# Kernel tuning notes

Hardware: AMD Instinct MI355X
Metric: run time of the kernel (lower is better)

Reference implementation:

```python
import jax, jax.numpy as jnp
import numpy as np

DIM = 512
HEADS = 8
DK = DIM // HEADS
MAX_LEN = 22118
EPS = 1e-5


def _layernorm(h, g, b):
    m = jnp.mean(h, axis=-1, keepdims=True)
    v = jnp.mean((h - m) ** 2, axis=-1, keepdims=True)
    return (h - m) / jnp.sqrt(v + EPS) * g + b


def setup_inputs() -> dict:
    key = jax.random.key(0)
    ks = jax.random.split(key, 16)
    B, S = 4, 2048
    xavier = lambda k, shp: jax.random.normal(k, shp, jnp.float32) * np.sqrt(2.0 / (shp[0] + shp[1]))
    return {
        "x": jax.random.normal(ks[0], (B, S, DIM), jnp.float32),
        "vis_data": jax.random.normal(ks[1], (B, S, DIM), jnp.float32),
        "coord1": jax.random.randint(ks[2], (B, S), 0, MAX_LEN, jnp.int32),
        "coord2": jax.random.randint(ks[3], (B, S), 0, MAX_LEN, jnp.int32),
        "emb1": jax.random.normal(ks[4], (MAX_LEN, DIM // 2), jnp.float32) * 0.02,
        "emb2": jax.random.normal(ks[5], (MAX_LEN, DIM // 2), jnp.float32) * 0.02,
        "wq": xavier(ks[6], (DIM, DIM)), "bq": jnp.zeros((DIM,), jnp.float32),
        "wk": xavier(ks[7], (DIM, DIM)), "bk": jnp.zeros((DIM,), jnp.float32),
        "wv": xavier(ks[8], (DIM, DIM)), "bv": jnp.zeros((DIM,), jnp.float32),
        "w1": xavier(ks[9], (DIM, DIM)), "b1": jnp.zeros((DIM,), jnp.float32),
        "g1": jnp.ones((DIM,), jnp.float32), "beta1": jnp.zeros((DIM,), jnp.float32),
        "w2": xavier(ks[10], (DIM, DIM)), "b2": jnp.zeros((DIM,), jnp.float32),
        "g2": jnp.ones((DIM,), jnp.float32), "beta2": jnp.zeros((DIM,), jnp.float32),
    }


def reference(x, vis_data, coord1, coord2, emb1, emb2, wq, bq, wk, bk, wv, bv,
              w1, b1, g1, beta1, w2, b2, g2, beta2):
    B, S, _ = x.shape
    # learned positional encoding: concat of two coordinate embeddings
    pos = jnp.concatenate([emb1[coord1], emb2[coord2]], axis=-1)  # [B,S,DIM]
    xp = x + pos
    # Q/K from vis_data, V from position-encoded x
    q = (vis_data @ wq + bq).reshape(B, S, HEADS, DK)
    k = (vis_data @ wk + bk).reshape(B, S, HEADS, DK)
    v = (xp @ wv + bv).reshape(B, S, HEADS, DK)
    scores = jnp.einsum("bqhd,bkhd->bhqk", q, k) / np.sqrt(DK).astype(np.float32)
    attn = jax.nn.softmax(scores, axis=-1)  # dropout is identity in eval
    out = jnp.einsum("bhqk,bkhd->bqhd", attn, v).reshape(B, S, DIM)
    # post-attention MLP stack (self.layer)
    h = jax.nn.leaky_relu(out @ w1 + b1, negative_slope=0.2)
    h = _layernorm(h, g1, beta1)
    h = jax.nn.leaky_relu(h @ w2 + b2, negative_slope=0.2)
    h = _layernorm(h, g2, beta2)
    return h
```

## Files before the change

kernel.cpp:

```cpp
#include <hip/hip_runtime.h>

#define DIM 512
#define SEQ 2048
#define MROWS 8192

typedef short short8 __attribute__((ext_vector_type(8)));
typedef float floatx4 __attribute__((ext_vector_type(4)));

__device__ __forceinline__ ushort f2bf(float f) {
  union { float f; unsigned u; } v; v.f = f;
  unsigned r = v.u + 0x7fff + ((v.u >> 16) & 1);
  return (ushort)(r >> 16);
}
__device__ __forceinline__ float bf2f(ushort u) {
  union { unsigned u; float f; } v; v.u = ((unsigned)u) << 16;
  return v.f;
}
__device__ __forceinline__ float fast_exp2(float x) {
  float r;
  asm("v_exp_f32 %0, %1" : "=v"(r) : "v"(x));
  return r;
}

__global__ __launch_bounds__(256) void prep_wtrans_kernel(
    const float* __restrict__ x, const float* __restrict__ vis,
    const int* __restrict__ c1, const int* __restrict__ c2,
    const float* __restrict__ e1, const float* __restrict__ e2,
    const float* __restrict__ wq, const float* __restrict__ wk,
    const float* __restrict__ wv, const float* __restrict__ w1,
    const float* __restrict__ w2,
    ushort* __restrict__ xp_bf, ushort* __restrict__ vis_bf,
    ushort* __restrict__ wt_qkv, ushort* __restrict__ wt1,
    ushort* __restrict__ wt2) {
  __shared__ float Ls[64 * 65];
  if (blockIdx.x < 4096) {
    int gid = blockIdx.x * 256 + threadIdx.x;
    int row = gid >> 7;
    int col = (gid & 127) * 4;
    float4 vv = *(const float4*)(vis + (size_t)row * 512 + col);
    ushort4 vb; vb.x = f2bf(vv.x); vb.y = f2bf(vv.y); vb.z = f2bf(vv.z); vb.w = f2bf(vv.w);
    *(ushort4*)(vis_bf + (size_t)row * 512 + col) = vb;
    float4 p;
    if (col < 256) p = *(const float4*)(e1 + (size_t)c1[row] * 256 + col);
    else           p = *(const float4*)(e2 + (size_t)c2[row] * 256 + col - 256);
    float4 xv = *(const float4*)(x + (size_t)row * 512 + col);
    ushort4 xb; xb.x = f2bf(xv.x + p.x); xb.y = f2bf(xv.y + p.y);
    xb.z = f2bf(xv.z + p.z); xb.w = f2bf(xv.w + p.w);
    *(ushort4*)(xp_bf + (size_t)row * 512 + col) = xb;
  } else {
    int bid = blockIdx.x - 4096;
    int mid = bid >> 6;
    int tile = bid & 63;
    int k0 = (tile >> 3) * 64, n0 = (tile & 7) * 64;
    const float* W = mid == 0 ? wq : mid == 1 ? wk : mid == 2 ? wv : mid == 3 ? w1 : w2;
    ushort* outp = mid < 3 ? (wt_qkv + (size_t)mid * 512 * 512) : (mid == 3 ? wt1 : wt2);
    float scale = (mid == 0) ? 0.125f * 1.44269504f : 1.0f;
    int r = threadIdx.x >> 4, c4 = (threadIdx.x & 15) * 4;
#pragma unroll
    for (int i = 0; i < 4; i++) {
      int row = i * 16 + r;
      float4 wv4 = *(const float4*)(W + (size_t)(k0 + row) * 512 + n0 + c4);
      Ls[row * 65 + c4 + 0] = wv4.x * scale;
      Ls[row * 65 + c4 + 1] = wv4.y * scale;
      Ls[row * 65 + c4 + 2] = wv4.z * scale;
      Ls[row * 65 + c4 + 3] = wv4.w * scale;
    }
    __syncthreads();
    int n = threadIdx.x >> 2, kc = (threadIdx.x & 3) * 16;
    ushort pk[16];
#pragma unroll
    for (int i = 0; i < 16; i++) pk[i] = f2bf(Ls[(kc + i) * 65 + n]);
    ushort* op = outp + (size_t)(n0 + n) * 512 + k0 + kc;
    *(uint4*)op = *(uint4*)pk;
    *(uint4*)(op + 8) = *(uint4*)(pk + 8);
  }
}

template <bool LEAKY>
__global__ __launch_bounds__(256, 4) void gemm_mfma(
    const ushort* __restrict__ A01, const ushort* __restrict__ A2,
    const ushort* __restrict__ Wt,
    const float* __restrict__ bias0, const float* __restrict__ bias1,
    const float* __restrict__ bias2,
    ushort* __restrict__ out0, ushort* __restrict__ out1,
    ushort* __restrict__ out2, float s0scale) {
  __shared__ __align__(16) ushort Sm[24576];
  int t = threadIdx.x;
  int seg = blockIdx.x >> 2;
  int nloc0 = (blockIdx.x & 3) * 128;
  int n0w = blockIdx.x * 128;
  int m0 = blockIdx.y * 64;
  const ushort* A = (seg < 2) ? A01 : A2;
  const float* bias = seg == 0 ? bias0 : seg == 1 ? bias1 : bias2;
  ushort* out = seg == 0 ? out0 : seg == 1 ? out1 : out2;
  float bscale = seg == 0 ? s0scale : 1.0f;

  int w = t >> 6, lane = t & 63;
  int wm = (w & 1) * 32, wn = (w >> 1) * 64;
  int quad = lane >> 4, lcol = lane & 15;
  int l8g = lane >> 3, l7g = lane & 7;
  int gchs = (l7g ^ l8g) * 8;

  floatx4 acc[2][4] = {};

#define GEMM_STAGE(K0, BUF)                                                   \
  {                                                                           \
    ushort* As_ = Sm + (BUF) * 12288;                                         \
    ushort* Bs_ = As_ + 4096;                                                 \
    _Pragma("unroll") for (int i = 0; i < 2; i++) {                           \
      int r0 = w * 16 + i * 8;                                                \
      __builtin_amdgcn_global_load_lds(                                       \
          (const __attribute__((address_space(1))) unsigned*)(                \
              A + (size_t)(m0 + r0 + l8g) * 512 + (K0) + gchs),               \
          (__attribute__((address_space(3))) unsigned*)(&As_[r0 * 64]),       \
          16, 0, 0);                                                          \
    }                                                                         \
    _Pragma("unroll") for (int i = 0; i < 4; i++) {                           \
      int r0 = w * 32 + i * 8;                                                \
      __builtin_amdgcn_global_load_lds(                                       \
          (const __attribute__((address_space(1))) unsigned*)(                \
              Wt + (size_t)(n0w + r0 + l8g) * 512 + (K0) + gchs),             \
          (__attribute__((address_space(3))) unsigned*)(&Bs_[r0 * 64]),       \
          16, 0, 0);                                                          \
    }                                                                         \
  }

  GEMM_STAGE(0, 0);
  asm volatile("s_waitcnt vmcnt(0)" ::: "memory");
  __syncthreads();

  for (int ks = 0; ks < 8; ks++) {
    int cur = ks & 1;
    if (ks < 7) GEMM_STAGE((ks + 1) * 64, cur ^ 1);
    const ushort* As = Sm + cur * 12288;
    const ushort* Bs = As + 4096;
#pragma unroll
    for (int kc = 0; kc < 2; kc++) {
      int pch = ((kc * 4 + quad) ^ (lcol & 7)) * 8;
      short8 af[2], bfr[4];
#pragma unroll
      for (int i = 0; i < 2; i++)
        af[i] = *(const short8*)(&As[(wm + i * 16 + lcol) * 64 + pch]);
#pragma unroll
      for (int i = 0; i < 4; i++)
        bfr[i] = *(const short8*)(&Bs[(wn + i * 16 + lcol) * 64 + pch]);
#pragma unroll
      for (int mt = 0; mt < 2; mt++)
#pragma unroll
        for (int nt = 0; nt < 4; nt++)
          acc[mt][nt] = __builtin_amdgcn_mfma_f32_16x16x32_bf16(
              af[mt], bfr[nt], acc[mt][nt], 0, 0, 0);
    }
    asm volatile("s_waitcnt vmcnt(0)" ::: "memory");
    __syncthreads();
  }
#undef GEMM_STAGE

  float* Ls = (float*)Sm + w * 1088;
  int rr = lane >> 2, cc = (lane & 3) * 16;
#pragma unroll
  for (int mt = 0; mt < 2; mt++) {
#pragma unroll
    for (int nt = 0; nt < 4; nt++) {
      float bv = bias[nloc0 + wn + nt * 16 + lcol] * bscale;
#pragma unroll
      for (int r = 0; r < 4; r++) {
        float vv = acc[mt][nt][r] + bv;
        if (LEAKY) vv = vv >= 0.f ? vv : 0.2f * vv;
        Ls[(quad * 4 + r) * 68 + nt * 16 + lcol] = vv;
      }
    }
    asm volatile("s_waitcnt lgkmcnt(0)" ::: "memory");
    ushort pk[16];
#pragma unroll
    for (int i = 0; i < 16; i += 4) {
      float4 fv = *(const float4*)(&Ls[rr * 68 + cc + i]);
      pk[i] = f2bf(fv.x); pk[i + 1] = f2bf(fv.y);
      pk[i + 2] = f2bf(fv.z); pk[i + 3] = f2bf(fv.w);
    }
    ushort* op = out + (size_t)(m0 + wm + mt * 16 + rr) * 512 + nloc0 + wn + cc;
    *(uint4*)op = *(uint4*)pk;
    *(uint4*)(op + 8) = *(uint4*)(pk + 8);
    asm volatile("s_waitcnt lgkmcnt(0)" ::: "memory");
  }
}

__global__ __launch_bounds__(256, 4) void attn_mfma_kernel(
    const ushort* __restrict__ q, const ushort* __restrict__ k,
    const ushort* __restrict__ v, ushort* __restrict__ out) {
  __shared__ __align__(16) ushort Ks[2][64 * 64];
  __shared__ __align__(16) ushort Vt[2][64 * 64];
  __shared__ __align__(16) unsigned Pp[2048];
  int t = threadIdx.x;
  int blk = blockIdx.x;
  blk = ((blk & 7) << 7) | (blk >> 3);
  int qt = blk & 31, h = (blk >> 5) & 7, b = blk >> 8;
  int wave = t >> 6, lane = t & 63, quad = lane >> 4, lcol = lane & 15;
  int q0 = qt * 64 + wave * 16;
  const size_t base = (size_t)b * SEQ * 512 + h * 64;

  short8 qf[2];
#pragma unroll
  for (int kc = 0; kc < 2; kc++)
    qf[kc] = *(const short8*)(
        q + base + (size_t)(q0 + lcol) * 512 + kc * 32 + quad * 8);

  floatx4 O[4] = {};
  float lsum = 0.f;

  unsigned* Ppw = Pp + wave * 512;
  int l8 = lane >> 3, l7 = lane & 7;
  int kchs = (l7 ^ l8) * 8;
  int krow = wave * 8 + l8;
  int vp = t & 31, vdg = t >> 5;
  const ushort* vbase = v + base + (size_t)(2 * vp) * 512 + vdg * 8;

  uint4 ka0, ka1, va, vb;

  ka0 = *(const uint4*)(k + base + (size_t)krow * 512 + kchs);
  ka1 = *(const uint4*)(k + base + (size_t)(krow + 32) * 512 + kchs);
  va = *(const uint4*)vbase;
  vb = *(const uint4*)(vbase + 512);
  *(uint4*)(&Ks[0][krow * 64 + l7 * 8]) = ka0;
  *(uint4*)(&Ks[0][(krow + 32) * 64 + l7 * 8]) = ka1;
  {
    const ushort* a0 = (const ushort*)&va;
    const ushort* a1 = (const ushort*)&vb;
#pragma unroll
    for (int i = 0; i < 8; i++) {
      int dim = vdg * 8 + i;
      unsigned pack = (unsigned)a0[i] | ((unsigned)a1[i] << 16);
      *(unsigned*)(&Vt[0][dim * 64 + ((vp >> 2) ^ (dim & 7)) * 8 +
                          (vp & 3) * 2]) = pack;
    }
  }
  __syncthreads();

  int cb = 0;
  for (int it = 0; it < 32; it++) {
    if (it < 31) {
      int ktn = (it + 1) * 64;
      ka0 = *(const uint4*)(k + base + (size_t)(ktn + krow) * 512 + kchs);
      ka1 = *(const uint4*)(k + base + (size_t)(ktn + krow + 32) * 512 + kchs);
      const ushort* vr = vbase + (size_t)ktn * 512;
      va = *(const uint4*)vr;
      vb = *(const uint4*)(vr + 512);
    }

    const ushort* Ksb = Ks[cb];
    const ushort* Vtb = Vt[cb];

    short8 kf[2][4];
#pragma unroll
    for (int kc = 0; kc < 2; kc++) {
      int pch = ((kc * 4 + quad) ^ l7) * 8;
#pragma unroll
      for (int jt = 0; jt < 4; jt++)
        kf[kc][jt] = *(const short8*)(&Ksb[(jt * 16 + lcol) * 64 + pch]);
    }
    floatx4 S[4] = {};
    __builtin_amdgcn_s_setprio(1);
#pragma unroll
    for (int kc = 0; kc < 2; kc++)
#pragma unroll
      for (int jt = 0; jt < 4; jt++)
        S[jt] = __builtin_amdgcn_mfma_f32_16x16x32_bf16(
            kf[kc][jt], qf[kc], S[jt], 0, 0, 0);
    __builtin_amdgcn_s_setprio(0);

#pragma unroll
    for (int jt = 0; jt < 4; jt++) {
      float e0 = fast_exp2(S[jt][0]);
      float e1 = fast_exp2(S[jt][1]);
      float e2 = fast_exp2(S[jt][2]);
      float e3 = fast_exp2(S[jt][3]);
      lsum += (e0 + e1) + (e2 + e3);
      unsigned p0, p1;
      asm("v_cvt_pk_bf16_f32 %0, %1, %2" : "=v"(p0) : "v"(e0), "v"(e1));
      asm("v_cvt_pk_bf16_f32 %0, %1, %2" : "=v"(p1) : "v"(e2), "v"(e3));
      int c0 = 2 * jt + (quad >> 1);
      uint2 pk2; pk2.x = p0; pk2.y = p1;
      *(uint2*)(Ppw + lcol * 32 + ((c0 ^ l7) << 2) + (quad & 1) * 2) = pk2;
    }
    asm volatile("s_waitcnt lgkmcnt(0)" ::: "memory");

#pragma unroll
    for (int kc = 0; kc < 2; kc++) {
      short8 vf[4];
      int ch = ((kc * 4 + quad) ^ l7) * 8;
#pragma unroll
      for (int nt = 0; nt < 4; nt++)
        vf[nt] = *(const short8*)(&Vtb[(nt * 16 + lcol) * 64 + ch]);
      short8 pf = *(const short8*)(Ppw + lcol * 32 +
                                   (((kc * 4 + quad) ^ l7) << 2));
      __builtin_amdgcn_s_setprio(1);
#pragma unroll
      for (int nt = 0; nt < 4; nt++)
        O[nt] = __builtin_amdgcn_mfma_f32_16x16x32_bf16(
            vf[nt], pf, O[nt], 0, 0, 0);
      __builtin_amdgcn_s_setprio(0);
    }

    if (it < 31) {
      ushort* Ksn = Ks[cb ^ 1];
      *(uint4*)(&Ksn[krow * 64 + l7 * 8]) = ka0;
      *(uint4*)(&Ksn[(krow + 32) * 64 + l7 * 8]) = ka1;
      const ushort* a0 = (const ushort*)&va;
      const ushort* a1 = (const ushort*)&vb;
      ushort* Vtn = Vt[cb ^ 1];
#pragma unroll
      for (int i = 0; i < 8; i++) {
        int dim = vdg * 8 + i;
        unsigned pack = (unsigned)a0[i] | ((unsigned)a1[i] << 16);
        *(unsigned*)(&Vtn[dim * 64 + ((vp >> 2) ^ (dim & 7)) * 8 +
                          (vp & 3) * 2]) = pack;
      }
    }
    __syncthreads();
    cb ^= 1;
  }

  lsum += __shfl_xor(lsum, 16, 64);
  lsum += __shfl_xor(lsum, 32, 64);
  float rl = 1.f / lsum;
#pragma unroll
  for (int nt = 0; nt < 4; nt++) {
    ushort4 o;
    o.x = f2bf(O[nt][0] * rl);
    o.y = f2bf(O[nt][1] * rl);
    o.z = f2bf(O[nt][2] * rl);
    o.w = f2bf(O[nt][3] * rl);
    *(ushort4*)(out + base + (size_t)(q0 + lcol) * 512 + nt * 16 + quad * 4) = o;
  }
}

template <bool OUTF32>
__global__ __launch_bounds__(256) void ln_kernel(
    const ushort* __restrict__ h, const float* __restrict__ g,
    const float* __restrict__ beta, void* __restrict__ outv) {
  int wave = threadIdx.x >> 6, lane = threadIdx.x & 63;
  int row = blockIdx.x * 4 + wave;
  uint4 raw = *(const uint4*)(h + (size_t)row * 512 + lane * 8);
  const ushort* hu = (const ushort*)&raw;
  float vals[8];
#pragma unroll
  for (int i = 0; i < 8; i++) vals[i] = bf2f(hu[i]);
  float sum = 0.f;
#pragma unroll
  for (int i = 0; i < 8; i++) sum += vals[i];
#pragma unroll
  for (int off = 32; off >= 1; off >>= 1) sum += __shfl_xor(sum, off, 64);
  float mean = sum * (1.f / 512.f);
  float vs = 0.f;
#pragma unroll
  for (int i = 0; i < 8; i++) { float d = vals[i] - mean; vs += d * d; }
#pragma unroll
  for (int off = 32; off >= 1; off >>= 1) vs += __shfl_xor(vs, off, 64);
  float rstd = rsqrtf(vs * (1.f / 512.f) + 1e-5f);
  float4 gv0 = *(const float4*)(g + lane * 8);
  float4 gv1 = *(const float4*)(g + lane * 8 + 4);
  float4 bv0 = *(const float4*)(beta + lane * 8);
  float4 bv1 = *(const float4*)(beta + lane * 8 + 4);
  float gr[8] = {gv0.x, gv0.y, gv0.z, gv0.w, gv1.x, gv1.y, gv1.z, gv1.w};
  float br[8] = {bv0.x, bv0.y, bv0.z, bv0.w, bv1.x, bv1.y, bv1.z, bv1.w};
  float res[8];
#pragma unroll
  for (int i = 0; i < 8; i++) res[i] = (vals[i] - mean) * rstd * gr[i] + br[i];
  if (OUTF32) {
    float* op = (float*)outv + (size_t)row * 512 + lane * 8;
    float4 o0, o1;
    o0.x = res[0]; o0.y = res[1]; o0.z = res[2]; o0.w = res[3];
    o1.x = res[4]; o1.y = res[5]; o1.z = res[6]; o1.w = res[7];
    *(float4*)op = o0; *(float4*)(op + 4) = o1;
  } else {
    ushort* op = (ushort*)outv + (size_t)row * 512 + lane * 8;
    ushort4 o0, o1;
    o0.x = f2bf(res[0]); o0.y = f2bf(res[1]); o0.z = f2bf(res[2]); o0.w = f2bf(res[3]);
    o1.x = f2bf(res[4]); o1.y = f2bf(res[5]); o1.z = f2bf(res[6]); o1.w = f2bf(res[7]);
    *(ushort4*)op = o0; *(ushort4*)(op + 4) = o1;
  }
}

extern "C" void kernel_launch(void* const* d_in, const int* in_sizes, int n_in,
                              void* d_out, int out_size, void* d_ws,
                              size_t ws_size, hipStream_t stream) {
  (void)in_sizes; (void)n_in; (void)out_size; (void)ws_size;
  const float* x     = (const float*)d_in[0];
  const float* vis   = (const float*)d_in[1];
  const int*   c1    = (const int*)d_in[2];
  const int*   c2    = (const int*)d_in[3];
  const float* e1    = (const float*)d_in[4];
  const float* e2    = (const float*)d_in[5];
  const float* wq    = (const float*)d_in[6];
  const float* bq    = (const float*)d_in[7];
  const float* wk    = (const float*)d_in[8];
  const float* bk    = (const float*)d_in[9];
  const float* wv    = (const float*)d_in[10];
  const float* bv    = (const float*)d_in[11];
  const float* w1    = (const float*)d_in[12];
  const float* b1    = (const float*)d_in[13];
  const float* g1    = (const float*)d_in[14];
  const float* beta1 = (const float*)d_in[15];
  const float* w2    = (const float*)d_in[16];
  const float* b2    = (const float*)d_in[17];
  const float* g2    = (const float*)d_in[18];
  const float* beta2 = (const float*)d_in[19];
  float* out = (float*)d_out;
  ushort* ws = (ushort*)d_ws;

  const size_t BUF = (size_t)MROWS * 512;
  ushort* xp_bf  = ws;
  ushort* vis_bf = ws + BUF;
  ushort* q_bf   = ws + 2 * BUF;
  ushort* k_bf   = ws + 3 * BUF;
  ushort* v_bf   = ws + 4 * BUF;
  ushort* wt_qkv = ws + 5 * BUF;
  ushort* wt1    = wt_qkv + 1536 * 512;
  ushort* wt2    = wt1 + 512 * 512;
  ushort* attn_bf = vis_bf;
  ushort* h1_bf   = xp_bf;
  ushort* ln1_bf  = q_bf;
  ushort* h2_bf   = k_bf;

  prep_wtrans_kernel<<<4416, 256, 0, stream>>>(
      x, vis, c1, c2, e1, e2, wq, wk, wv, w1, w2, xp_bf, vis_bf, wt_qkv, wt1, wt2);
  gemm_mfma<false><<<dim3(12, 128), 256, 0, stream>>>(
      vis_bf, xp_bf, wt_qkv, bq, bk, bv, q_bf, k_bf, v_bf, 0.125f * 1.44269504f);
  attn_mfma_kernel<<<1024, 256, 0, stream>>>(q_bf, k_bf, v_bf, attn_bf);
  gemm_mfma<true><<<dim3(4, 128), 256, 0, stream>>>(
      attn_bf, attn_bf, wt1, b1, b1, b1, h1_bf, h1_bf, h1_bf, 1.0f);
  ln_kernel<false><<<2048, 256, 0, stream>>>(h1_bf, g1, beta1, ln1_bf);
  gemm_mfma<true><<<dim3(4, 128), 256, 0, stream>>>(
      ln1_bf, ln1_bf, wt2, b2, b2, b2, h2_bf, h2_bf, h2_bf, 1.0f);
  ln_kernel<true><<<2048, 256, 0, stream>>>(h2_bf, g2, beta2, out);
}
```

Before: 248.2 us.

## Enlarge GEMM tile to 128x128 and drop double buffering

The GEMM kernel's M tile grows from 64 to 128 rows, so each wave now computes a 64x64 output block with 4x4 accumulators and the grid halves along M. The LDS double buffer is replaced by a single buffer, with a wait and barrier before each k-step's compute. The aim is more operand reuse per loaded tile and fewer blocks. In exchange, global loads no longer overlap with MFMA work, register pressure rises (launch bounds go from 4 to 3), and the three GEMMs launch fewer blocks (768 and 256).

After: 260.7 us. +5.0%, slower.

```diff
diff --git a/kernel.cpp b/kernel.cpp
--- a/kernel.cpp
+++ b/kernel.cpp
@@ -77,89 +77,80 @@
 }
 
 template <bool LEAKY>
-__global__ __launch_bounds__(256, 4) void gemm_mfma(
+__global__ __launch_bounds__(256, 3) void gemm_mfma(
     const ushort* __restrict__ A01, const ushort* __restrict__ A2,
     const ushort* __restrict__ Wt,
     const float* __restrict__ bias0, const float* __restrict__ bias1,
     const float* __restrict__ bias2,
     ushort* __restrict__ out0, ushort* __restrict__ out1,
     ushort* __restrict__ out2, float s0scale) {
-  __shared__ __align__(16) ushort Sm[24576];
+  __shared__ __align__(16) ushort Sm[16384];
+  ushort* As = Sm;
+  ushort* Bs = Sm + 8192;
   int t = threadIdx.x;
   int seg = blockIdx.x >> 2;
   int nloc0 = (blockIdx.x & 3) * 128;
   int n0w = blockIdx.x * 128;
-  int m0 = blockIdx.y * 64;
+  int m0 = blockIdx.y * 128;
   const ushort* A = (seg < 2) ? A01 : A2;
   const float* bias = seg == 0 ? bias0 : seg == 1 ? bias1 : bias2;
   ushort* out = seg == 0 ? out0 : seg == 1 ? out1 : out2;
   float bscale = seg == 0 ? s0scale : 1.0f;
 
   int w = t >> 6, lane = t & 63;
-  int wm = (w & 1) * 32, wn = (w >> 1) * 64;
+  int wm = (w & 1) * 64, wn = (w >> 1) * 64;
   int quad = lane >> 4, lcol = lane & 15;
   int l8g = lane >> 3, l7g = lane & 7;
   int gchs = (l7g ^ l8g) * 8;
 
-  floatx4 acc[2][4] = {};
-
-#define GEMM_STAGE(K0, BUF)                                                   \
-  {                                                                           \
-    ushort* As_ = Sm + (BUF) * 12288;                                         \
-    ushort* Bs_ = As_ + 4096;                                                 \
-    _Pragma("unroll") for (int i = 0; i < 2; i++) {                           \
-      int r0 = w * 16 + i * 8;                                                \
-      __builtin_amdgcn_global_load_lds(                                       \
-          (const __attribute__((address_space(1))) unsigned*)(                \
-              A + (size_t)(m0 + r0 + l8g) * 512 + (K0) + gchs),               \
-          (__attribute__((address_space(3))) unsigned*)(&As_[r0 * 64]),       \
-          16, 0, 0);                                                          \
-    }                                                                         \
-    _Pragma("unroll") for (int i = 0; i < 4; i++) {                           \
-      int r0 = w * 32 + i * 8;                                                \
-      __builtin_amdgcn_global_load_lds(                                       \
-          (const __attribute__((address_space(1))) unsigned*)(                \
-              Wt + (size_t)(n0w + r0 + l8g) * 512 + (K0) + gchs),             \
-          (__attribute__((address_space(3))) unsigned*)(&Bs_[r0 * 64]),       \
-          16, 0, 0);                                                          \
-    }                                                                         \
-  }
-
-  GEMM_STAGE(0, 0);
-  asm volatile("s_waitcnt vmcnt(0)" ::: "memory");
-  __syncthreads();
+  floatx4 acc[4][4] = {};
 
   for (int ks = 0; ks < 8; ks++) {
-    int cur = ks & 1;
-    if (ks < 7) GEMM_STAGE((ks + 1) * 64, cur ^ 1);
-    const ushort* As = Sm + cur * 12288;
-    const ushort* Bs = As + 4096;
+    int k0 = ks * 64;
+#pragma unroll
+    for (int i = 0; i < 4; i++) {
+      int r0 = w * 32 + i * 8;
+      __builtin_amdgcn_global_load_lds(
+          (const __attribute__((address_space(1))) unsigned*)(
+              A + (size_t)(m0 + r0 + l8g) * 512 + k0 + gchs),
+          (__attribute__((address_space(3))) unsigned*)(&As[r0 * 64]),
+          16, 0, 0);
+    }
+#pragma unroll
+    for (int i = 0; i < 4; i++) {
+      int r0 = w * 32 + i * 8;
+      __builtin_amdgcn_global_load_lds(
+          (const __attribute__((address_space(1))) unsigned*)(
+              Wt + (size_t)(n0w + r0 + l8g) * 512 + k0 + gchs),
+          (__attribute__((address_space(3))) unsigned*)(&Bs[r0 * 64]),
+          16, 0, 0);
+    }
+    asm volatile("s_waitcnt vmcnt(0)" ::: "memory");
+    __syncthreads();
 #pragma unroll
     for (int kc = 0; kc < 2; kc++) {
       int pch = ((kc * 4 + quad) ^ (lcol & 7)) * 8;
-      short8 af[2], bfr[4];
-#pragma unroll
-      for (int i = 0; i < 2; i++)
+      short8 af[4], bfr[4];
+#pragma unroll
+      for (int i = 0; i < 4; i++)
         af[i] = *(const short8*)(&As[(wm + i * 16 + lcol) * 64 + pch]);
 #pragma unroll
       for (int i = 0; i < 4; i++)
         bfr[i] = *(const short8*)(&Bs[(wn + i * 16 + lcol) * 64 + pch]);
 #pragma unroll
-      for (int mt = 0; mt < 2; mt++)
+      for (int mt = 0; mt < 4; mt++)
 #pragma unroll
         for (int nt = 0; nt < 4; nt++)
           acc[mt][nt] = __builtin_amdgcn_mfma_f32_16x16x32_bf16(
               af[mt], bfr[nt], acc[mt][nt], 0, 0, 0);
     }
-    asm volatile("s_waitcnt vmcnt(0)" ::: "memory");
     __syncthreads();
   }
-#undef GEMM_STAGE
 
   float* Ls = (float*)Sm + w * 1088;
   int rr = lane >> 2, cc = (lane & 3) * 16;
 #pragma unroll
-  for (int mt = 0; mt < 2; mt++) {
+  for (int mt = 0; mt < 4; mt++) {
 #pragma unroll
     for (int nt = 0; nt < 4; nt++) {
       float bv = bias[nloc0 + wn + nt * 16 + lcol] * bscale;
@@ -424,13 +415,13 @@
 
   prep_wtrans_kernel<<<4416, 256, 0, stream>>>(
       x, vis, c1, c2, e1, e2, wq, wk, wv, w1, w2, xp_bf, vis_bf, wt_qkv, wt1, wt2);
-  gemm_mfma<false><<<dim3(12, 128), 256, 0, stream>>>(
+  gemm_mfma<false><<<dim3(12, 64), 256, 0, stream>>>(
       vis_bf, xp_bf, wt_qkv, bq, bk, bv, q_bf, k_bf, v_bf, 0.125f * 1.44269504f);
   attn_mfma_kernel<<<1024, 256, 0, stream>>>(q_bf, k_bf, v_bf, attn_bf);
-  gemm_mfma<true><<<dim3(4, 128), 256, 0, stream>>>(
+  gemm_mfma<true><<<dim3(4, 64), 256, 0, stream>>>(
       attn_bf, attn_bf, wt1, b1, b1, b1, h1_bf, h1_bf, h1_bf, 1.0f);
   ln_kernel<false><<<2048, 256, 0, stream>>>(h1_bf, g1, beta1, ln1_bf);
-  gemm_mfma<true><<<dim3(4, 128), 256, 0, stream>>>(
+  gemm_mfma<true><<<dim3(4, 64), 256, 0, stream>>>(
       ln1_bf, ln1_bf, wt2, b2, b2, b2, h2_bf, h2_bf, h2_bf, 1.0f);
   ln_kernel<true><<<2048, 256, 0, stream>>>(h2_bf, g2, beta2, out);
 }
```

## Fuse first layernorm into GEMM epilogue stats and next GEMM A-load

Applied to the files above, without the earlier changes.

Removes the standalone first layernorm kernel. The first MLP GEMM epilogue now accumulates per-row sum and sum-of-squares via shuffles and atomics into a stats buffer, which the prep kernel zeroes. The second GEMM normalizes its A tile on the fly from those stats while loading into shared memory. This saves a kernel launch and a full read/write pass of the activation. In exchange the A load moves from async global-to-LDS to synchronous register loads, and variance is computed as E[x²]−mean² in fp32.

New measurement: 254.1 us. +2.4%, slower.

```diff
diff --git a/kernel.cpp b/kernel.cpp
--- a/kernel.cpp
+++ b/kernel.cpp
@@ -31,7 +31,7 @@
     const float* __restrict__ w2,
     ushort* __restrict__ xp_bf, ushort* __restrict__ vis_bf,
     ushort* __restrict__ wt_qkv, ushort* __restrict__ wt1,
-    ushort* __restrict__ wt2) {
+    ushort* __restrict__ wt2, float* __restrict__ stats) {
   __shared__ float Ls[64 * 65];
   if (blockIdx.x < 4096) {
     int gid = blockIdx.x * 256 + threadIdx.x;
@@ -47,6 +47,10 @@
     ushort4 xb; xb.x = f2bf(xv.x + p.x); xb.y = f2bf(xv.y + p.y);
     xb.z = f2bf(xv.z + p.z); xb.w = f2bf(xv.w + p.w);
     *(ushort4*)(xp_bf + (size_t)row * 512 + col) = xb;
+  } else if (blockIdx.x >= 4416) {
+    int idx = (blockIdx.x - 4416) * 256 + threadIdx.x;
+    float2 z; z.x = 0.f; z.y = 0.f;
+    *(float2*)(stats + idx * 2) = z;
   } else {
     int bid = blockIdx.x - 4096;
     int mid = bid >> 6;
@@ -76,14 +80,16 @@
   }
 }
 
-template <bool LEAKY>
+template <int MODE>
 __global__ __launch_bounds__(256, 4) void gemm_mfma(
     const ushort* __restrict__ A01, const ushort* __restrict__ A2,
     const ushort* __restrict__ Wt,
     const float* __restrict__ bias0, const float* __restrict__ bias1,
     const float* __restrict__ bias2,
     ushort* __restrict__ out0, ushort* __restrict__ out1,
-    ushort* __restrict__ out2, float s0scale) {
+    ushort* __restrict__ out2, float s0scale,
+    float* __restrict__ stats, const float* __restrict__ lng,
+    const float* __restrict__ lnb) {
   __shared__ __align__(16) ushort Sm[24576];
   int t = threadIdx.x;
   int seg = blockIdx.x >> 2;
@@ -93,7 +99,7 @@
   const ushort* A = (seg < 2) ? A01 : A2;
   const float* bias = seg == 0 ? bias0 : seg == 1 ? bias1 : bias2;
   ushort* out = seg == 0 ? out0 : seg == 1 ? out1 : out2;
-  float bscale = seg == 0 ? s0scale : 1.0f;
+  float bscale = (MODE == 0 && seg == 0) ? s0scale : 1.0f;
 
   int w = t >> 6, lane = t & 63;
   int wm = (w & 1) * 32, wn = (w >> 1) * 64;
@@ -101,19 +107,54 @@
   int l8g = lane >> 3, l7g = lane & 7;
   int gchs = (l7g ^ l8g) * 8;
 
+  float amean[2] = {0.f, 0.f}, arstd[2] = {0.f, 0.f};
+  if constexpr (MODE == 2) {
+#pragma unroll
+    for (int i = 0; i < 2; i++) {
+      int row = m0 + w * 16 + i * 8 + l8g;
+      float s0 = stats[row * 2], s1 = stats[row * 2 + 1];
+      float mean = s0 * (1.f / 512.f);
+      float var = s1 * (1.f / 512.f) - mean * mean;
+      amean[i] = mean;
+      arstd[i] = rsqrtf(var + 1e-5f);
+    }
+  }
+
   floatx4 acc[2][4] = {};
 
 #define GEMM_STAGE(K0, BUF)                                                   \
   {                                                                           \
     ushort* As_ = Sm + (BUF) * 12288;                                         \
     ushort* Bs_ = As_ + 4096;                                                 \
-    _Pragma("unroll") for (int i = 0; i < 2; i++) {                           \
-      int r0 = w * 16 + i * 8;                                                \
-      __builtin_amdgcn_global_load_lds(                                       \
-          (const __attribute__((address_space(1))) unsigned*)(                \
-              A + (size_t)(m0 + r0 + l8g) * 512 + (K0) + gchs),               \
-          (__attribute__((address_space(3))) unsigned*)(&As_[r0 * 64]),       \
-          16, 0, 0);                                                          \
+    if constexpr (MODE == 2) {                                                \
+      _Pragma("unroll") for (int i = 0; i < 2; i++) {                         \
+        int rl = w * 16 + i * 8 + l8g;                                        \
+        uint4 rawv = *(const uint4*)(A + (size_t)(m0 + rl) * 512 + (K0) +     \
+                                     l7g * 8);                                \
+        float4 gl0 = *(const float4*)(lng + (K0) + l7g * 8);                  \
+        float4 gl1 = *(const float4*)(lng + (K0) + l7g * 8 + 4);              \
+        float4 bl0 = *(const float4*)(lnb + (K0) + l7g * 8);                  \
+        float4 bl1 = *(const float4*)(lnb + (K0) + l7g * 8 + 4);              \
+        const ushort* hv = (const ushort*)&rawv;                              \
+        float gr2[8] = {gl0.x, gl0.y, gl0.z, gl0.w,                           \
+                        gl1.x, gl1.y, gl1.z, gl1.w};                          \
+        float br2[8] = {bl0.x, bl0.y, bl0.z, bl0.w,                           \
+                        bl1.x, bl1.y, bl1.z, bl1.w};                          \
+        ushort pk8[8];                                                        \
+        _Pragma("unroll") for (int e = 0; e < 8; e++)                         \
+          pk8[e] = f2bf((bf2f(hv[e]) - amean[i]) * arstd[i] * gr2[e] +        \
+                        br2[e]);                                              \
+        *(uint4*)(&As_[rl * 64 + ((l7g ^ l8g) * 8)]) = *(uint4*)pk8;          \
+      }                                                                       \
+    } else {                                                                  \
+      _Pragma("unroll") for (int i = 0; i < 2; i++) {                         \
+        int r0 = w * 16 + i * 8;                                              \
+        __builtin_amdgcn_global_load_lds(                                     \
+            (const __attribute__((address_space(1))) unsigned*)(              \
+                A + (size_t)(m0 + r0 + l8g) * 512 + (K0) + gchs),             \
+            (__attribute__((address_space(3))) unsigned*)(&As_[r0 * 64]),     \
+            16, 0, 0);                                                        \
+      }                                                                       \
     }                                                                         \
     _Pragma("unroll") for (int i = 0; i < 4; i++) {                           \
       int r0 = w * 32 + i * 8;                                                \
@@ -160,14 +201,32 @@
   int rr = lane >> 2, cc = (lane & 3) * 16;
 #pragma unroll
   for (int mt = 0; mt < 2; mt++) {
+    float rs[4] = {0.f, 0.f, 0.f, 0.f}, rq[4] = {0.f, 0.f, 0.f, 0.f};
 #pragma unroll
     for (int nt = 0; nt < 4; nt++) {
       float bv = bias[nloc0 + wn + nt * 16 + lcol] * bscale;
 #pragma unroll
       for (int r = 0; r < 4; r++) {
         float vv = acc[mt][nt][r] + bv;
-        if (LEAKY) vv = vv >= 0.f ? vv : 0.2f * vv;
+        if (MODE >= 1) vv = vv >= 0.f ? vv : 0.2f * vv;
+        if constexpr (MODE == 1) { rs[r] += vv; rq[r] += vv * vv; }
         Ls[(quad * 4 + r) * 68 + nt * 16 + lcol] = vv;
+      }
+    }
+    if constexpr (MODE == 1) {
+#pragma unroll
+      for (int r = 0; r < 4; r++) {
+        float s = rs[r], q = rq[r];
+#pragma unroll
+        for (int m = 1; m <= 8; m <<= 1) {
+          s += __shfl_xor(s, m, 64);
+          q += __shfl_xor(q, m, 64);
+        }
+        if (lcol == 0) {
+          int row = m0 + wm + mt * 16 + quad * 4 + r;
+          atomicAdd(&stats[row * 2], s);
+          atomicAdd(&stats[row * 2 + 1], q);
+        }
       }
     }
     asm volatile("s_waitcnt lgkmcnt(0)" ::: "memory");
@@ -417,20 +476,23 @@
   ushort* wt_qkv = ws + 5 * BUF;
   ushort* wt1    = wt_qkv + 1536 * 512;
   ushort* wt2    = wt1 + 512 * 512;
+  float*  stats  = (float*)(wt2 + 512 * 512);
   ushort* attn_bf = vis_bf;
   ushort* h1_bf   = xp_bf;
-  ushort* ln1_bf  = q_bf;
   ushort* h2_bf   = k_bf;
 
-  prep_wtrans_kernel<<<4416, 256, 0, stream>>>(
-      x, vis, c1, c2, e1, e2, wq, wk, wv, w1, w2, xp_bf, vis_bf, wt_qkv, wt1, wt2);
-  gemm_mfma<false><<<dim3(12, 128), 256, 0, stream>>>(
-      vis_bf, xp_bf, wt_qkv, bq, bk, bv, q_bf, k_bf, v_bf, 0.125f * 1.44269504f);
+  prep_wtrans_kernel<<<4448, 256, 0, stream>>>(
+      x, vis, c1, c2, e1, e2, wq, wk, wv, w1, w2, xp_bf, vis_bf, wt_qkv, wt1,
+      wt2, stats);
+  gemm_mfma<0><<<dim3(12, 128), 256, 0, stream>>>(
+      vis_bf, xp_bf, wt_qkv, bq, bk, bv, q_bf, k_bf, v_bf,
+      0.125f * 1.44269504f, nullptr, nullptr, nullptr);
   attn_mfma_kernel<<<1024, 256, 0, stream>>>(q_bf, k_bf, v_bf, attn_bf);
-  gemm_mfma<true><<<dim3(4, 128), 256, 0, stream>>>(
-      attn_bf, attn_bf, wt1, b1, b1, b1, h1_bf, h1_bf, h1_bf, 1.0f);
-  ln_kernel<false><<<2048, 256, 0, stream>>>(h1_bf, g1, beta1, ln1_bf);
-  gemm_mfma<true><<<dim3(4, 128), 256, 0, stream>>>(
-      ln1_bf, ln1_bf, wt2, b2, b2, b2, h2_bf, h2_bf, h2_bf, 1.0f);
+  gemm_mfma<1><<<dim3(4, 128), 256, 0, stream>>>(
+      attn_bf, attn_bf, wt1, b1, b1, b1, h1_bf, h1_bf, h1_bf, 1.0f,
+      stats, nullptr, nullptr);
+  gemm_mfma<2><<<dim3(4, 128), 256, 0, stream>>>(
+      h1_bf, h1_bf, wt2, b2, b2, b2, h2_bf, h2_bf, h2_bf, 1.0f,
+      stats, g1, beta1);
   ln_kernel<true><<<2048, 256, 0, stream>>>(h2_bf, g2, beta2, out);
 }
```
